# Kernel tuning notes

Hardware: AMD Instinct MI355X
Metric: run time of the kernel (lower is better)

The kernel has to match this reference:

```python
import jax, jax.numpy as jnp
import numpy as np

EMB = 512       # emb_dim
H = 8           # n_heads
HD = EMB // H   # head_dim = 64
FREQ = 64       # freq_features
PERIOD = 0.1
N = 2048


def setup_inputs() -> dict:
    key = jax.random.key(0)
    ks = jax.random.split(key, 6)
    x = jax.random.normal(ks[0], (1, N, EMB), dtype=jnp.float32)
    v = jax.random.normal(ks[1], (1, N, 3), dtype=jnp.float32)
    vec_map = v / jnp.linalg.norm(v, axis=-1, keepdims=True)  # unit direction vectors
    s_in = 1.0 / np.sqrt(EMB)
    W_qkv = jax.random.normal(ks[2], (EMB, 3 * EMB), dtype=jnp.float32) * s_in
    b_qkv = jnp.zeros((3 * EMB,), dtype=jnp.float32)
    W_bias = jax.random.normal(ks[3], (FREQ, H), dtype=jnp.float32) * (1.0 / np.sqrt(FREQ))
    b_bias = jnp.zeros((H,), dtype=jnp.float32)
    W_out = jax.random.normal(ks[4], (EMB, EMB), dtype=jnp.float32) * s_in
    b_out = jnp.zeros((EMB,), dtype=jnp.float32)
    return {"x": x, "vec_map": vec_map, "W_qkv": W_qkv, "b_qkv": b_qkv,
            "W_bias": W_bias, "b_bias": b_bias, "W_out": W_out, "b_out": b_out}


def reference(x, vec_map, W_qkv, b_qkv, W_bias, b_bias, W_out, b_out):
    batch_dim = x.shape[:-2]
    n = x.shape[-2]
    # QKV projection -> (*, N, H, 3, HD)
    qkv = (x @ W_qkv + b_qkv).reshape(*batch_dim, n, H, 3, HD)
    q, k, v = (qkv[..., 0, :], qkv[..., 1, :], qkv[..., 2, :])
    # attention scores (*, Q, K, H), softmax over the K axis (axis=-2)
    attn = jnp.einsum('...qht,...kht->...qkh', q, k) / np.sqrt(HD)
    attn = jax.nn.softmax(attn, axis=-2)
    # relative bias from pairwise angles between direction vectors
    dot = jnp.einsum('...nc,...mc->...nm', vec_map, vec_map)
    angle = jnp.arccos(jnp.clip(dot, 0.0, 1.0)) / 0.001
    freqs = jnp.linspace(0.0, 1.0, FREQ // 2, dtype=jnp.float32) / PERIOD
    phase = freqs * angle[..., None]                      # (*, N, N, FREQ/2)
    pos = jnp.concatenate((jnp.sin(phase), jnp.cos(phase)), axis=-1)  # (*, N, N, FREQ)
    bias = pos @ W_bias + b_bias                          # (*, N, N, H)
    attn = attn + bias
    # weighted sum of values -> (*, N, EMB)
    y = jnp.einsum('...qkh,...kht->...qht', attn, v).reshape(*batch_dim, n, EMB)
    return y @ W_out + b_out
```

## Files before the change

kernel.cpp:

```cpp
#include <hip/hip_runtime.h>
#include <hip/hip_bf16.h>
#include <math.h>

#define NT 2048
#define EMBD 512
#define NH 8
#define QKV_LD 1536
#define KSPLIT 4

typedef unsigned short u16;
typedef __attribute__((ext_vector_type(8))) short short8;
typedef __attribute__((ext_vector_type(4))) float v4f;

static __device__ __forceinline__ float bf2f(unsigned int u) {
    union { unsigned int i; float f; } c; c.i = u << 16; return c.f;
}
static __device__ __forceinline__ unsigned int f2bf(float x) {
    union { float f; unsigned int u; } c; c.f = x;
    return (c.u + 0x7fffu + ((c.u >> 16) & 1u)) >> 16;
}

__global__ __launch_bounds__(256) void split_x(const float* __restrict__ x,
    u16* __restrict__ xh, u16* __restrict__ xl)
{
    int i = (blockIdx.x * 256 + threadIdx.x) << 2;
    float4 v = *(const float4*)(x + i);
    float f[4] = {v.x, v.y, v.z, v.w};
    unsigned int hi[4], lo[4];
#pragma unroll
    for (int j = 0; j < 4; ++j) {
        hi[j] = f2bf(f[j]);
        lo[j] = f2bf(f[j] - bf2f(hi[j]));
    }
    uint2 wh; wh.x = hi[0] | (hi[1] << 16); wh.y = hi[2] | (hi[3] << 16);
    uint2 wl; wl.x = lo[0] | (lo[1] << 16); wl.y = lo[2] | (lo[3] << 16);
    *(uint2*)(xh + i) = wh;
    *(uint2*)(xl + i) = wl;
}

__global__ __launch_bounds__(256) void split_wt(const float* __restrict__ W,
    u16* __restrict__ wth, u16* __restrict__ wtl, int ld)
{
    __shared__ float tile[64][65];
    const int n0 = blockIdx.x << 6, k0 = blockIdx.y << 6;
    const int t = threadIdx.x;
    const int r = t >> 2, c4 = (t & 3) << 4;
#pragma unroll
    for (int j = 0; j < 4; ++j)
        *(float4*)&tile[r][c4 + (j << 2)] =
            *(const float4*)(W + (size_t)(k0 + r) * ld + n0 + c4 + (j << 2));
    __syncthreads();
    const int n_l = t >> 2;
    u16 th[16], tl[16];
#pragma unroll
    for (int j = 0; j < 16; ++j) {
        float f = tile[c4 + j][n_l];
        unsigned int h = f2bf(f);
        th[j] = (u16)h;
        tl[j] = (u16)f2bf(f - bf2f(h));
    }
    u16* dh = wth + (size_t)(n0 + n_l) * EMBD + k0 + c4;
    u16* dl = wtl + (size_t)(n0 + n_l) * EMBD + k0 + c4;
    *(uint4*)dh       = *(uint4*)&th[0];
    *(uint4*)(dh + 8) = *(uint4*)&th[8];
    *(uint4*)dl       = *(uint4*)&tl[0];
    *(uint4*)(dl + 8) = *(uint4*)&tl[8];
}

__global__ __launch_bounds__(256) void gemm_qkv_mfma(const u16* __restrict__ xh,
    const u16* __restrict__ xl, const u16* __restrict__ wth,
    const u16* __restrict__ wtl, const float* __restrict__ bias,
    u16* __restrict__ qkvb)
{
    const int n0 = blockIdx.x << 6, m0 = blockIdx.y << 6;
    const int w = threadIdx.x >> 6, lane = threadIdx.x & 63;
    const int wm = w >> 1, wn = w & 1;
    const int fr = lane & 15, kd = (lane >> 4) << 3;

    const u16* ah0 = xh + (size_t)(m0 + wm * 32 + fr) * EMBD + kd;
    const u16* al0 = xl + (size_t)(m0 + wm * 32 + fr) * EMBD + kd;
    const u16* bh0 = wth + (size_t)(n0 + wn * 32 + fr) * EMBD + kd;
    const u16* bl0 = wtl + (size_t)(n0 + wn * 32 + fr) * EMBD + kd;

    v4f acc[2][2] = {};
    for (int kc = 0; kc < EMBD; kc += 32) {
        short8 a_h[2], a_l[2], b_h[2], b_l[2];
#pragma unroll
        for (int im = 0; im < 2; ++im) {
            a_h[im] = *(const short8*)(ah0 + (size_t)im * 16 * EMBD + kc);
            a_l[im] = *(const short8*)(al0 + (size_t)im * 16 * EMBD + kc);
        }
#pragma unroll
        for (int in = 0; in < 2; ++in) {
            b_h[in] = *(const short8*)(bh0 + (size_t)in * 16 * EMBD + kc);
            b_l[in] = *(const short8*)(bl0 + (size_t)in * 16 * EMBD + kc);
        }
#pragma unroll
        for (int im = 0; im < 2; ++im)
#pragma unroll
            for (int in = 0; in < 2; ++in) {
                acc[im][in] = __builtin_amdgcn_mfma_f32_16x16x32_bf16(a_h[im], b_h[in], acc[im][in], 0, 0, 0);
                acc[im][in] = __builtin_amdgcn_mfma_f32_16x16x32_bf16(a_h[im], b_l[in], acc[im][in], 0, 0, 0);
                acc[im][in] = __builtin_amdgcn_mfma_f32_16x16x32_bf16(a_l[im], b_h[in], acc[im][in], 0, 0, 0);
            }
    }
    const int qr = (lane >> 4) << 2;
#pragma unroll
    for (int im = 0; im < 2; ++im)
#pragma unroll
        for (int in = 0; in < 2; ++in) {
            int n = n0 + wn * 32 + in * 16 + fr;
            float bv = bias[n];
#pragma unroll
            for (int r = 0; r < 4; ++r) {
                int m = m0 + wm * 32 + im * 16 + qr + r;
                qkvb[(size_t)m * QKV_LD + n] = (u16)f2bf(acc[im][in][r] + bv);
            }
        }
}

__global__ __launch_bounds__(256) void transpose_v(const u16* __restrict__ qkvb,
                                                   u16* __restrict__ Vt)
{
    __shared__ u16 tile[64][72];
    const int h = blockIdx.y, k0 = blockIdx.x << 6;
    const int t = threadIdx.x;
    {
        int r = t >> 2, cg = (t & 3) << 4;
        const u16* src = qkvb + (size_t)(k0 + r) * QKV_LD + h * 192 + 128 + cg;
        *(uint4*)&tile[r][cg]     = *(const uint4*)src;
        *(uint4*)&tile[r][cg + 8] = *(const uint4*)(src + 8);
    }
    __syncthreads();
    {
        int c = t >> 2, kg = (t & 3) << 4;
        u16 tmp[16];
#pragma unroll
        for (int j = 0; j < 16; ++j) tmp[j] = tile[kg + j][c];
        u16* dst = Vt + ((size_t)h * 64 + c) * NT + k0 + kg;
        *(uint4*)dst       = *(uint4*)&tmp[0];
        *(uint4*)(dst + 8) = *(uint4*)&tmp[8];
    }
}

__global__ __launch_bounds__(512, 2) void fused_attn(
    const u16* __restrict__ qkvb, const u16* __restrict__ Vt,
    const float* __restrict__ vec, const float* __restrict__ Wb,
    const float* __restrict__ bb, float* __restrict__ zpart,
    float* __restrict__ partsP, float* __restrict__ partsB)
{
    __shared__ float flds[32];
    __shared__ float vql[96];
    __shared__ float ang[32 * 65];
    __shared__ u16 tile[8 * 2056];

    const int bid = blockIdx.x;
    const int xcd = bid & 7;
    const int zsp = xcd >> 1;
    const int qt  = ((bid >> 3) << 1) | (xcd & 1);
    const int q0 = qt << 5;
    const int kbase = zsp << 9;

    const int t = threadIdx.x;
    const int w = t >> 6;
    const int lane = t & 63;
    const int fr = lane & 15;
    const int hi4 = lane >> 4;
    const int kd = hi4 << 3;
    const int qr = hi4 << 2;

    if (t < 32) flds[t] = __fdiv_rn(__fdiv_rn((float)t, 31.0f), 0.1f);
    else if (t < 128) vql[t - 32] = vec[q0 * 3 + (t - 32)];

    short8 BS, BC;
#pragma unroll
    for (int j = 0; j < 8; ++j) {
        float ws = (fr < 8) ? Wb[(kd + j) * 8 + fr] : 0.0f;
        float wc = (fr < 8) ? Wb[(32 + kd + j) * 8 + fr] : 0.0f;
        BS[j] = (short)f2bf(ws);
        BC[j] = (short)f2bf(wc);
    }
    const float bbv = (fr < 8) ? bb[fr] : 0.0f;

    short8 aq[2][2];
#pragma unroll
    for (int mb = 0; mb < 2; ++mb)
#pragma unroll
        for (int kk = 0; kk < 2; ++kk)
            aq[mb][kk] = *(const short8*)(qkvb +
                (size_t)(q0 + mb * 16 + fr) * QKV_LD + w * 192 + kk * 32 + kd);

    v4f accP[2][4] = {};
    v4f accB[2][4] = {};
    float zacc[2][4] = {};

    __syncthreads();

    for (int c = 0; c < 8; ++c) {
        const int kc = kbase + (c << 6);
        {
            const int p0 = t << 2;
            const int q = p0 >> 6;
            const int kl = p0 & 63;
            const float a0 = vql[q * 3], a1 = vql[q * 3 + 1], a2 = vql[q * 3 + 2];
            const float* vk = vec + (size_t)(kc + kl) * 3;
#pragma unroll
            for (int j = 0; j < 4; ++j) {
                float c0 = vk[j * 3], c1 = vk[j * 3 + 1], c2 = vk[j * 3 + 2];
                float dot = __fadd_rn(__fadd_rn(__fmul_rn(a0, c0), __fmul_rn(a1, c1)),
                                      __fmul_rn(a2, c2));
                float dotc = fminf(fmaxf(dot, 0.0f), 1.0f);
                ang[q * 65 + kl + j] = __fdiv_rn(acosf(dotc), 0.001f);
            }
        }
        __syncthreads();
#pragma unroll
        for (int gi = 0; gi < 16; ++gi) {
            const int g = w + (gi << 3);
            const int q = g >> 2;
            const int ksub = (g & 3) << 4;
            const float av = ang[q * 65 + ksub + fr];
            short8 AS, AC;
#pragma unroll
            for (int j = 0; j < 8; ++j) {
                float ph = __fmul_rn(flds[kd + j], av);
                float rv = ph * 0.15915494309189535f;
                float rf = rv - floorf(rv);
                AS[j] = (short)f2bf(__builtin_amdgcn_sinf(rf));
                AC[j] = (short)f2bf(__builtin_amdgcn_cosf(rf));
            }
            v4f cb = {};
            cb = __builtin_amdgcn_mfma_f32_16x16x32_bf16(AS, BS, cb, 0, 0, 0);
            cb = __builtin_amdgcn_mfma_f32_16x16x32_bf16(AC, BC, cb, 0, 0, 0);
            if (fr < 8) {
                const int kg = (ksub + qr) >> 3;
                unsigned int pk0 = f2bf(cb[0] + bbv) | (f2bf(cb[1] + bbv) << 16);
                unsigned int pk1 = f2bf(cb[2] + bbv) | (f2bf(cb[3] + bbv) << 16);
                uint2 wv; wv.x = pk0; wv.y = pk1;
                *(uint2*)&tile[fr * 2056 + q * 64 + ((kg ^ (q & 7)) << 3) + (qr & 7)] = wv;
            }
        }
        __syncthreads();
        short8 vb[4][2], bk[4][2];
#pragma unroll
        for (int nt = 0; nt < 4; ++nt)
#pragma unroll
            for (int kk = 0; kk < 2; ++kk) {
                vb[nt][kk] = *(const short8*)(Vt +
                    (size_t)(w * 64 + nt * 16 + fr) * NT + kc + kk * 32 + kd);
                bk[nt][kk] = *(const short8*)(qkvb +
                    (size_t)(kc + nt * 16 + fr) * QKV_LD + w * 192 + 64 + kk * 32 + kd);
            }
#pragma unroll
        for (int mb = 0; mb < 2; ++mb) {
            const int q = mb * 16 + fr;
#pragma unroll
            for (int kk = 0; kk < 2; ++kk) {
                short8 ab = *(const short8*)&tile[w * 2056 + q * 64 +
                    (((kk * 4 + hi4) ^ (q & 7)) << 3)];
#pragma unroll
                for (int nt = 0; nt < 4; ++nt)
                    accB[mb][nt] = __builtin_amdgcn_mfma_f32_16x16x32_bf16(ab, vb[nt][kk], accB[mb][nt], 0, 0, 0);
            }
        }
        v4f sacc[2][4] = {};
#pragma unroll
        for (int mb = 0; mb < 2; ++mb)
#pragma unroll
            for (int nt = 0; nt < 4; ++nt) {
                sacc[mb][nt] = __builtin_amdgcn_mfma_f32_16x16x32_bf16(aq[mb][0], bk[nt][0], sacc[mb][nt], 0, 0, 0);
                sacc[mb][nt] = __builtin_amdgcn_mfma_f32_16x16x32_bf16(aq[mb][1], bk[nt][1], sacc[mb][nt], 0, 0, 0);
            }
        unsigned int pk[2][4][2];
#pragma unroll
        for (int mb = 0; mb < 2; ++mb)
#pragma unroll
            for (int nt = 0; nt < 4; ++nt)
#pragma unroll
                for (int r2 = 0; r2 < 2; ++r2) {
                    float e0 = __expf(sacc[mb][nt][2 * r2] * 0.125f);
                    float e1 = __expf(sacc[mb][nt][2 * r2 + 1] * 0.125f);
                    zacc[mb][2 * r2] += e0;
                    zacc[mb][2 * r2 + 1] += e1;
                    pk[mb][nt][r2] = f2bf(e0) | (f2bf(e1) << 16);
                }
        __syncthreads();
#pragma unroll
        for (int mb = 0; mb < 2; ++mb)
#pragma unroll
            for (int nt = 0; nt < 4; ++nt) {
                const int kg = (nt << 1) + (fr >> 3);
#pragma unroll
                for (int r = 0; r < 4; ++r) {
                    const int q = mb * 16 + qr + r;
                    tile[w * 2056 + q * 64 + ((kg ^ (q & 7)) << 3) + (fr & 7)] =
                        (u16)(pk[mb][nt][r >> 1] >> ((r & 1) << 4));
                }
            }
        __syncthreads();
#pragma unroll
        for (int mb = 0; mb < 2; ++mb) {
            const int q = mb * 16 + fr;
#pragma unroll
            for (int kk = 0; kk < 2; ++kk) {
                short8 ap = *(const short8*)&tile[w * 2056 + q * 64 +
                    (((kk * 4 + hi4) ^ (q & 7)) << 3)];
#pragma unroll
                for (int nt = 0; nt < 4; ++nt)
                    accP[mb][nt] = __builtin_amdgcn_mfma_f32_16x16x32_bf16(ap, vb[nt][kk], accP[mb][nt], 0, 0, 0);
            }
        }
    }
#pragma unroll
    for (int off = 1; off < 16; off <<= 1)
#pragma unroll
        for (int mb = 0; mb < 2; ++mb)
#pragma unroll
            for (int r = 0; r < 4; ++r)
                zacc[mb][r] += __shfl_xor(zacc[mb][r], off);
    if (fr == 0) {
#pragma unroll
        for (int mb = 0; mb < 2; ++mb)
#pragma unroll
            for (int r = 0; r < 4; ++r)
                zpart[((size_t)zsp * 8 + w) * NT + q0 + mb * 16 + qr + r] = zacc[mb][r];
    }
    float* pP = partsP + (size_t)zsp * NT * EMBD;
    float* pB = partsB + (size_t)zsp * NT * EMBD;
#pragma unroll
    for (int mb = 0; mb < 2; ++mb)
#pragma unroll
        for (int nt = 0; nt < 4; ++nt)
#pragma unroll
            for (int r = 0; r < 4; ++r) {
                const size_t idx = (size_t)(q0 + mb * 16 + qr + r) * EMBD +
                                   (w << 6) + (nt << 4) + fr;
                pP[idx] = accP[mb][nt][r];
                pB[idx] = accB[mb][nt][r];
            }
}

__global__ __launch_bounds__(256) void reduce_y2(const float* __restrict__ partsP,
    const float* __restrict__ partsB, const float* __restrict__ zpart,
    u16* __restrict__ yh, u16* __restrict__ yl)
{
    const int MN = NT * EMBD;
    int i = (blockIdx.x * 256 + threadIdx.x) << 2;
    const int q = i >> 9;
    const int h = (i & 511) >> 6;
    float zs = 0.0f;
#pragma unroll
    for (int z = 0; z < KSPLIT; ++z) zs += zpart[((size_t)z * 8 + h) * NT + q];
    float4 aP = *(const float4*)(partsP + i);
    float4 aB = *(const float4*)(partsB + i);
#pragma unroll
    for (int z = 1; z < KSPLIT; ++z) {
        float4 p = *(const float4*)(partsP + (size_t)z * MN + i);
        float4 b = *(const float4*)(partsB + (size_t)z * MN + i);
        aP.x += p.x; aP.y += p.y; aP.z += p.z; aP.w += p.w;
        aB.x += b.x; aB.y += b.y; aB.z += b.z; aB.w += b.w;
    }
    const float iz = 1.0f / zs;
    float f[4] = {aP.x * iz + aB.x, aP.y * iz + aB.y,
                  aP.z * iz + aB.z, aP.w * iz + aB.w};
    unsigned int hi[4], lo[4];
#pragma unroll
    for (int j = 0; j < 4; ++j) {
        hi[j] = f2bf(f[j]);
        lo[j] = f2bf(f[j] - bf2f(hi[j]));
    }
    uint2 wh; wh.x = hi[0] | (hi[1] << 16); wh.y = hi[2] | (hi[3] << 16);
    uint2 wl; wl.x = lo[0] | (lo[1] << 16); wl.y = lo[2] | (lo[3] << 16);
    *(uint2*)(yh + i) = wh;
    *(uint2*)(yl + i) = wl;
}

__global__ __launch_bounds__(256) void gemm_out_mfma(const u16* __restrict__ yh,
    const u16* __restrict__ yl, const u16* __restrict__ wh,
    const u16* __restrict__ wl, const float* __restrict__ bias,
    float* __restrict__ out)
{
    const int n0 = blockIdx.x << 6, m0 = blockIdx.y << 6;
    const int w = threadIdx.x >> 6, lane = threadIdx.x & 63;
    const int wm = w >> 1, wn = w & 1;
    const int fr = lane & 15, kd = (lane >> 4) << 3;

    const u16* ah0 = yh + (size_t)(m0 + wm * 32 + fr) * EMBD + kd;
    const u16* al0 = yl + (size_t)(m0 + wm * 32 + fr) * EMBD + kd;
    const u16* bh0 = wh + (size_t)(n0 + wn * 32 + fr) * EMBD + kd;
    const u16* bl0 = wl + (size_t)(n0 + wn * 32 + fr) * EMBD + kd;

    v4f acc[2][2] = {};
    for (int kc = 0; kc < EMBD; kc += 32) {
        short8 a_h[2], a_l[2], b_h[2], b_l[2];
#pragma unroll
        for (int im = 0; im < 2; ++im) {
            a_h[im] = *(const short8*)(ah0 + (size_t)im * 16 * EMBD + kc);
            a_l[im] = *(const short8*)(al0 + (size_t)im * 16 * EMBD + kc);
        }
#pragma unroll
        for (int in = 0; in < 2; ++in) {
            b_h[in] = *(const short8*)(bh0 + (size_t)in * 16 * EMBD + kc);
            b_l[in] = *(const short8*)(bl0 + (size_t)in * 16 * EMBD + kc);
        }
#pragma unroll
        for (int im = 0; im < 2; ++im)
#pragma unroll
            for (int in = 0; in < 2; ++in) {
                acc[im][in] = __builtin_amdgcn_mfma_f32_16x16x32_bf16(a_h[im], b_h[in], acc[im][in], 0, 0, 0);
                acc[im][in] = __builtin_amdgcn_mfma_f32_16x16x32_bf16(a_h[im], b_l[in], acc[im][in], 0, 0, 0);
                acc[im][in] = __builtin_amdgcn_mfma_f32_16x16x32_bf16(a_l[im], b_h[in], acc[im][in], 0, 0, 0);
            }
    }
    const int qr = (lane >> 4) << 2;
#pragma unroll
    for (int im = 0; im < 2; ++im)
#pragma unroll
        for (int in = 0; in < 2; ++in) {
            int n = n0 + wn * 32 + in * 16 + fr;
            float bv = bias[n];
#pragma unroll
            for (int r = 0; r < 4; ++r) {
                int m = m0 + wm * 32 + im * 16 + qr + r;
                out[(size_t)m * EMBD + n] = acc[im][in][r] + bv;
            }
        }
}

extern "C" void kernel_launch(void* const* d_in, const int* in_sizes, int n_in,
                              void* d_out, int out_size, void* d_ws, size_t ws_size,
                              hipStream_t stream)
{
    const float* x    = (const float*)d_in[0];
    const float* vec  = (const float*)d_in[1];
    const float* Wqkv = (const float*)d_in[2];
    const float* bqkv = (const float*)d_in[3];
    const float* Wb   = (const float*)d_in[4];
    const float* bb   = (const float*)d_in[5];
    const float* Wout = (const float*)d_in[6];
    const float* bout = (const float*)d_in[7];
    float* out = (float*)d_out;

    char* ws = (char*)d_ws;
    u16*   qkvb   = (u16*)(ws);
    u16*   Vt     = (u16*)(ws + 6291456);
    float* zpart  = (float*)(ws + 8388608);
    float* partsP = (float*)(ws + 8650752);
    float* partsB = (float*)(ws + 25427968);
    u16*   yh     = (u16*)(ws + 42205184);
    u16*   yl     = (u16*)(ws + 44302336);
    u16*   xh     = (u16*)(ws + 46399488);
    u16*   xl     = (u16*)(ws + 48496640);
    u16*   wth    = (u16*)(ws + 50593792);
    u16*   wtl    = (u16*)(ws + 52166656);
    u16*   woth   = (u16*)(ws + 46399488);
    u16*   wotl   = (u16*)(ws + 46923776);

    split_x<<<1024, 256, 0, stream>>>(x, xh, xl);
    split_wt<<<dim3(24, 8), 256, 0, stream>>>(Wqkv, wth, wtl, QKV_LD);
    gemm_qkv_mfma<<<dim3(24, 32), 256, 0, stream>>>(xh, xl, wth, wtl, bqkv, qkvb);
    transpose_v<<<dim3(32, 8), 256, 0, stream>>>(qkvb, Vt);
    fused_attn<<<64 * KSPLIT, 512, 0, stream>>>(qkvb, Vt, vec, Wb, bb,
                                                zpart, partsP, partsB);
    reduce_y2<<<1024, 256, 0, stream>>>(partsP, partsB, zpart, yh, yl);
    split_wt<<<dim3(8, 8), 256, 0, stream>>>(Wout, woth, wotl, EMBD);
    gemm_out_mfma<<<dim3(8, 32), 256, 0, stream>>>(yh, yl, woth, wotl, bout, out);
}
```

Baseline: 264.9 us.

## Double attention key split, merge prep kernels, use packed bf16 converts

```diff
diff --git a/kernel.cpp b/kernel.cpp
--- a/kernel.cpp
+++ b/kernel.cpp
@@ -6,7 +6,7 @@
 #define EMBD 512
 #define NH 8
 #define QKV_LD 1536
-#define KSPLIT 4
+#define KSPLIT 8
 
 typedef unsigned short u16;
 typedef __attribute__((ext_vector_type(8))) short short8;
@@ -19,31 +19,41 @@
     union { float f; unsigned int u; } c; c.f = x;
     return (c.u + 0x7fffu + ((c.u >> 16) & 1u)) >> 16;
 }
-
-__global__ __launch_bounds__(256) void split_x(const float* __restrict__ x,
-    u16* __restrict__ xh, u16* __restrict__ xl)
-{
-    int i = (blockIdx.x * 256 + threadIdx.x) << 2;
-    float4 v = *(const float4*)(x + i);
-    float f[4] = {v.x, v.y, v.z, v.w};
-    unsigned int hi[4], lo[4];
-#pragma unroll
-    for (int j = 0; j < 4; ++j) {
-        hi[j] = f2bf(f[j]);
-        lo[j] = f2bf(f[j] - bf2f(hi[j]));
-    }
-    uint2 wh; wh.x = hi[0] | (hi[1] << 16); wh.y = hi[2] | (hi[3] << 16);
-    uint2 wl; wl.x = lo[0] | (lo[1] << 16); wl.y = lo[2] | (lo[3] << 16);
-    *(uint2*)(xh + i) = wh;
-    *(uint2*)(xl + i) = wl;
-}
-
-__global__ __launch_bounds__(256) void split_wt(const float* __restrict__ W,
-    u16* __restrict__ wth, u16* __restrict__ wtl, int ld)
+static __device__ __forceinline__ unsigned int cvtpk(float lo, float hi) {
+    unsigned int r;
+    asm("v_cvt_pk_bf16_f32 %0, %1, %2" : "=v"(r) : "v"(lo), "v"(hi));
+    return r;
+}
+
+__global__ __launch_bounds__(256) void prep(const float* __restrict__ x,
+    u16* __restrict__ xh, u16* __restrict__ xl,
+    const float* __restrict__ Wqkv, u16* __restrict__ wth, u16* __restrict__ wtl,
+    const float* __restrict__ Wout, u16* __restrict__ woth, u16* __restrict__ wotl)
 {
     __shared__ float tile[64][65];
-    const int n0 = blockIdx.x << 6, k0 = blockIdx.y << 6;
+    int b = blockIdx.x;
     const int t = threadIdx.x;
+    if (b < 1024) {
+        int i = (b * 256 + t) << 2;
+        float4 v = *(const float4*)(x + i);
+        float f[4] = {v.x, v.y, v.z, v.w};
+        unsigned int hi[4], lo[4];
+#pragma unroll
+        for (int j = 0; j < 4; ++j) {
+            hi[j] = f2bf(f[j]);
+            lo[j] = f2bf(f[j] - bf2f(hi[j]));
+        }
+        uint2 wh; wh.x = hi[0] | (hi[1] << 16); wh.y = hi[2] | (hi[3] << 16);
+        uint2 wl; wl.x = lo[0] | (lo[1] << 16); wl.y = lo[2] | (lo[3] << 16);
+        *(uint2*)(xh + i) = wh;
+        *(uint2*)(xl + i) = wl;
+        return;
+    }
+    b -= 1024;
+    const float* W; u16* th; u16* tl; int ld, bx, by;
+    if (b < 192) { W = Wqkv; th = wth;  tl = wtl;  ld = QKV_LD; bx = b % 24; by = b / 24; }
+    else { b -= 192; W = Wout; th = woth; tl = wotl; ld = EMBD; bx = b & 7; by = b >> 3; }
+    const int n0 = bx << 6, k0 = by << 6;
     const int r = t >> 2, c4 = (t & 3) << 4;
 #pragma unroll
     for (int j = 0; j < 4; ++j)
@@ -51,20 +61,20 @@
             *(const float4*)(W + (size_t)(k0 + r) * ld + n0 + c4 + (j << 2));
     __syncthreads();
     const int n_l = t >> 2;
-    u16 th[16], tl[16];
+    u16 vh[16], vl[16];
 #pragma unroll
     for (int j = 0; j < 16; ++j) {
         float f = tile[c4 + j][n_l];
         unsigned int h = f2bf(f);
-        th[j] = (u16)h;
-        tl[j] = (u16)f2bf(f - bf2f(h));
-    }
-    u16* dh = wth + (size_t)(n0 + n_l) * EMBD + k0 + c4;
-    u16* dl = wtl + (size_t)(n0 + n_l) * EMBD + k0 + c4;
-    *(uint4*)dh       = *(uint4*)&th[0];
-    *(uint4*)(dh + 8) = *(uint4*)&th[8];
-    *(uint4*)dl       = *(uint4*)&tl[0];
-    *(uint4*)(dl + 8) = *(uint4*)&tl[8];
+        vh[j] = (u16)h;
+        vl[j] = (u16)f2bf(f - bf2f(h));
+    }
+    u16* dh = th + (size_t)(n0 + n_l) * EMBD + k0 + c4;
+    u16* dl = tl + (size_t)(n0 + n_l) * EMBD + k0 + c4;
+    *(uint4*)dh       = *(uint4*)&vh[0];
+    *(uint4*)(dh + 8) = *(uint4*)&vh[8];
+    *(uint4*)dl       = *(uint4*)&vl[0];
+    *(uint4*)(dl + 8) = *(uint4*)&vl[8];
 }
 
 __global__ __launch_bounds__(256) void gemm_qkv_mfma(const u16* __restrict__ xh,
@@ -143,7 +153,7 @@
     }
 }
 
-__global__ __launch_bounds__(512, 2) void fused_attn(
+__global__ __launch_bounds__(512, 4) void fused_attn(
     const u16* __restrict__ qkvb, const u16* __restrict__ Vt,
     const float* __restrict__ vec, const float* __restrict__ Wb,
     const float* __restrict__ bb, float* __restrict__ zpart,
@@ -155,11 +165,10 @@
     __shared__ u16 tile[8 * 2056];
 
     const int bid = blockIdx.x;
-    const int xcd = bid & 7;
-    const int zsp = xcd >> 1;
-    const int qt  = ((bid >> 3) << 1) | (xcd & 1);
+    const int zsp = bid & 7;
+    const int qt  = bid >> 3;
     const int q0 = qt << 5;
-    const int kbase = zsp << 9;
+    const int kbase = zsp << 8;
 
     const int t = threadIdx.x;
     const int w = t >> 6;
@@ -196,7 +205,7 @@
 
     __syncthreads();
 
-    for (int c = 0; c < 8; ++c) {
+    for (int c = 0; c < 4; ++c) {
         const int kc = kbase + (c << 6);
         {
             const int p0 = t << 2;
@@ -220,23 +229,28 @@
             const int q = g >> 2;
             const int ksub = (g & 3) << 4;
             const float av = ang[q * 65 + ksub + fr];
-            short8 AS, AC;
+            float sv[8], cv[8];
 #pragma unroll
             for (int j = 0; j < 8; ++j) {
                 float ph = __fmul_rn(flds[kd + j], av);
                 float rv = ph * 0.15915494309189535f;
                 float rf = rv - floorf(rv);
-                AS[j] = (short)f2bf(__builtin_amdgcn_sinf(rf));
-                AC[j] = (short)f2bf(__builtin_amdgcn_cosf(rf));
-            }
+                sv[j] = __builtin_amdgcn_sinf(rf);
+                cv[j] = __builtin_amdgcn_cosf(rf);
+            }
+            union { uint4 u; short8 v; } As, Ac;
+            As.u.x = cvtpk(sv[0], sv[1]); As.u.y = cvtpk(sv[2], sv[3]);
+            As.u.z = cvtpk(sv[4], sv[5]); As.u.w = cvtpk(sv[6], sv[7]);
+            Ac.u.x = cvtpk(cv[0], cv[1]); Ac.u.y = cvtpk(cv[2], cv[3]);
+            Ac.u.z = cvtpk(cv[4], cv[5]); Ac.u.w = cvtpk(cv[6], cv[7]);
             v4f cb = {};
-            cb = __builtin_amdgcn_mfma_f32_16x16x32_bf16(AS, BS, cb, 0, 0, 0);
-            cb = __builtin_amdgcn_mfma_f32_16x16x32_bf16(AC, BC, cb, 0, 0, 0);
+            cb = __builtin_amdgcn_mfma_f32_16x16x32_bf16(As.v, BS, cb, 0, 0, 0);
+            cb = __builtin_amdgcn_mfma_f32_16x16x32_bf16(Ac.v, BC, cb, 0, 0, 0);
             if (fr < 8) {
                 const int kg = (ksub + qr) >> 3;
-                unsigned int pk0 = f2bf(cb[0] + bbv) | (f2bf(cb[1] + bbv) << 16);
-                unsigned int pk1 = f2bf(cb[2] + bbv) | (f2bf(cb[3] + bbv) << 16);
-                uint2 wv; wv.x = pk0; wv.y = pk1;
+                uint2 wv;
+                wv.x = cvtpk(cb[0] + bbv, cb[1] + bbv);
+                wv.y = cvtpk(cb[2] + bbv, cb[3] + bbv);
                 *(uint2*)&tile[fr * 2056 + q * 64 + ((kg ^ (q & 7)) << 3) + (qr & 7)] = wv;
             }
         }
@@ -282,7 +296,7 @@
                     float e1 = __expf(sacc[mb][nt][2 * r2 + 1] * 0.125f);
                     zacc[mb][2 * r2] += e0;
                     zacc[mb][2 * r2 + 1] += e1;
-                    pk[mb][nt][r2] = f2bf(e0) | (f2bf(e1) << 16);
+                    pk[mb][nt][r2] = cvtpk(e0, e1);
                 }
         __syncthreads();
 #pragma unroll
@@ -445,24 +459,22 @@
     u16*   qkvb   = (u16*)(ws);
     u16*   Vt     = (u16*)(ws + 6291456);
     float* zpart  = (float*)(ws + 8388608);
-    float* partsP = (float*)(ws + 8650752);
-    float* partsB = (float*)(ws + 25427968);
-    u16*   yh     = (u16*)(ws + 42205184);
-    u16*   yl     = (u16*)(ws + 44302336);
-    u16*   xh     = (u16*)(ws + 46399488);
-    u16*   xl     = (u16*)(ws + 48496640);
-    u16*   wth    = (u16*)(ws + 50593792);
-    u16*   wtl    = (u16*)(ws + 52166656);
-    u16*   woth   = (u16*)(ws + 46399488);
-    u16*   wotl   = (u16*)(ws + 46923776);
-
-    split_x<<<1024, 256, 0, stream>>>(x, xh, xl);
-    split_wt<<<dim3(24, 8), 256, 0, stream>>>(Wqkv, wth, wtl, QKV_LD);
+    float* partsP = (float*)(ws + 8912896);
+    float* partsB = (float*)(ws + 42467328);
+    u16*   yh     = (u16*)(ws + 76021760);
+    u16*   yl     = (u16*)(ws + 78118912);
+    u16*   xh     = (u16*)(ws + 80216064);
+    u16*   xl     = (u16*)(ws + 82313216);
+    u16*   wth    = (u16*)(ws + 84410368);
+    u16*   wtl    = (u16*)(ws + 85983232);
+    u16*   woth   = (u16*)(ws + 87556096);
+    u16*   wotl   = (u16*)(ws + 88080384);
+
+    prep<<<1280, 256, 0, stream>>>(x, xh, xl, Wqkv, wth, wtl, Wout, woth, wotl);
     gemm_qkv_mfma<<<dim3(24, 32), 256, 0, stream>>>(xh, xl, wth, wtl, bqkv, qkvb);
     transpose_v<<<dim3(32, 8), 256, 0, stream>>>(qkvb, Vt);
     fused_attn<<<64 * KSPLIT, 512, 0, stream>>>(qkvb, Vt, vec, Wb, bb,
                                                 zpart, partsP, partsB);
     reduce_y2<<<1024, 256, 0, stream>>>(partsP, partsB, zpart, yh, yl);
-    split_wt<<<dim3(8, 8), 256, 0, stream>>>(Wout, woth, wotl, EMBD);
     gemm_out_mfma<<<dim3(8, 32), 256, 0, stream>>>(yh, yl, woth, wotl, bout, out);
 }
```

New measurement: 350.9 us. 32.5% more time.
